# Kernel optimization log

Measured on AMD Instinct MI355X. Metric: run time of the kernel, lower is better.

Reference implementation:

```python
import jax, jax.numpy as jnp
import numpy as np

N, E, D = 50000, 800000, 128
NEG_SLOPE = 0.01  # torch LeakyReLU default


def _linear_params(key, fan_in, fan_out, bias=True):
    k1, k2 = jax.random.split(key)
    bound = 1.0 / np.sqrt(fan_in)
    W = jax.random.uniform(k1, (fan_in, fan_out), minval=-bound, maxval=bound, dtype=jnp.float32)
    if not bias:
        return W
    b = jax.random.uniform(k2, (fan_out,), minval=-bound, maxval=bound, dtype=jnp.float32)
    return W, b


def setup_inputs() -> dict:
    key = jax.random.key(0)
    ks = jax.random.split(key, 8)
    x = jax.random.normal(ks[0], (N, D), dtype=jnp.float32)
    edge_index = jax.random.randint(ks[1], (2, E), 0, N, dtype=jnp.int64)
    Wk, bk = _linear_params(ks[2], D, D)
    Wq, bq = _linear_params(ks[3], D, D)
    Wv, bv = _linear_params(ks[4], D, D)
    Wskip = _linear_params(ks[5], D, D, bias=False)  # lin_skip has bias=False
    b_conv = jnp.zeros((D,), dtype=jnp.float32)       # ResGatedGraphConv bias param
    Wlin, blin = _linear_params(ks[6], D, D)
    return {"x": x, "edge_index": edge_index, "Wk": Wk, "bk": bk, "Wq": Wq,
            "bq": bq, "Wv": Wv, "bv": bv, "Wskip": Wskip, "b_conv": b_conv,
            "Wlin": Wlin, "blin": blin}


def reference(x, edge_index, Wk, bk, Wq, bq, Wv, bv, Wskip, b_conv, Wlin, blin):
    src, dst = edge_index[0], edge_index[1]  # j -> i
    # dense projections on nodes (cheap), gather to edges (memory-bound)
    k = x @ Wk + bk          # [N, D] key of target
    q = x @ Wq + bq          # [N, D] query of source
    v = x @ Wv + bv          # [N, D] value of source
    gate = jax.nn.relu(k[dst] + q[src])      # act=ReLU() per module
    msg = gate * v[src]                       # [E, D]
    agg = jax.ops.segment_sum(msg, dst, num_segments=x.shape[0])  # scatter-add
    x1 = agg + x @ Wskip + b_conv            # root weight + bias
    x2 = jnp.where(x1 >= 0, x1, NEG_SLOPE * x1)  # LeakyReLU
    return x2 @ Wlin + blin
```

## Files before the change

kernel.cpp:

```cpp
#include <hip/hip_runtime.h>

#define DD 128

typedef __attribute__((ext_vector_type(8))) short bf16x8;
typedef __attribute__((ext_vector_type(4))) float f32x4;

__device__ inline unsigned short f2bf(float f) {
    unsigned int u = __float_as_uint(f);
    u += 0x7FFFu + ((u >> 16) & 1u);
    return (unsigned short)(u >> 16);
}
__device__ inline float bf2f(unsigned short s) {
    return __uint_as_float(((unsigned int)s) << 16);
}

template <typename T> __device__ inline T cvt(float f);
template <> __device__ inline float cvt<float>(float f) { return f; }
template <> __device__ inline unsigned short cvt<unsigned short>(float f) { return f2bf(f); }

template <typename T> __device__ inline float2 ld2(const T* p);
template <> __device__ inline float2 ld2<float>(const float* p) {
    return *reinterpret_cast<const float2*>(p);
}
template <> __device__ inline float2 ld2<unsigned short>(const unsigned short* p) {
    const ushort2 u = *reinterpret_cast<const ushort2*>(p);
    return make_float2(bf2f(u.x), bf2f(u.y));
}


__global__ __launch_bounds__(256) void split_w_kernel(
    const float* __restrict__ W0, const float* __restrict__ W1,
    const float* __restrict__ W2, const float* __restrict__ W3,
    const float* __restrict__ W4,
    unsigned short* __restrict__ whi)
{
    const int idx = blockIdx.x * 256 + threadIdx.x;
    if (idx >= 5 * 2048) return;
    const int mat  = idx >> 11;
    const int rem  = idx & 2047;
    const int ks   = rem >> 9;
    const int nt   = (rem >> 6) & 7;
    const int lane = rem & 63;
    const int lr = lane & 15, lg = lane >> 4;
    const float* __restrict__ W = mat == 0 ? W0 : mat == 1 ? W1 : mat == 2 ? W2
                                 : mat == 3 ? W3 : W4;
    const int n = nt * 16 + lr;
    bf16x8 h8;
#pragma unroll
    for (int r = 0; r < 8; ++r) {
        const int k = ks * 32 + lg * 8 + r;
        h8[r] = (short)f2bf(W[k * DD + n]);
    }
    *reinterpret_cast<bf16x8*>(&whi[(long)idx * 8]) = h8;
}

template <bool XFORM>
__device__ inline void stage_rows512(const float* __restrict__ src,
                                     const float* __restrict__ addv,
                                     int row0, int N, int t,
                                     unsigned short* __restrict__ ldsA)
{
    const int m  = t >> 3;
    const int gr = row0 + m;
#pragma unroll
    for (int j = 0; j < 2; ++j) {
        const int o = (t & 7) + j * 8;
        float v[8];
        if (gr < N) {
            const float4 a = *reinterpret_cast<const float4*>(&src[(long)gr * DD + o * 8]);
            const float4 b = *reinterpret_cast<const float4*>(&src[(long)gr * DD + o * 8 + 4]);
            v[0] = a.x; v[1] = a.y; v[2] = a.z; v[3] = a.w;
            v[4] = b.x; v[5] = b.y; v[6] = b.z; v[7] = b.w;
        } else {
#pragma unroll
            for (int e = 0; e < 8; ++e) v[e] = 0.f;
        }
        if (XFORM) {
#pragma unroll
            for (int e = 0; e < 8; ++e) {
                const float s = v[e] + addv[o * 8 + e];
                v[e] = s >= 0.f ? s : 0.01f * s;
            }
        }
        bf16x8 h8;
#pragma unroll
        for (int e = 0; e < 8; ++e) h8[e] = (short)f2bf(v[e]);
        const int rt   = m >> 4;
        const int ks   = o >> 2;
        const int lane = (m & 15) + (o & 3) * 16;
        const int base = ((rt * 4 + ks) * 64 + lane) * 8;
        *reinterpret_cast<bf16x8*>(&ldsA[base]) = h8;
    }
}

__global__ __launch_bounds__(512) void proj_mfma_kernel(
    const float* __restrict__ x,
    const unsigned short* __restrict__ whi,
    const float* __restrict__ bk, const float* __restrict__ bq,
    const float* __restrict__ bv,
    float* __restrict__ kbuf, unsigned short* __restrict__ qvpk,
    float* __restrict__ agg, int* __restrict__ deg, int N)
{
    __shared__ unsigned short ldsA[16 * 64 * 8];
    const int t = threadIdx.x;
    const int row0 = blockIdx.x * 64;

    const int gid = blockIdx.x * 512 + t;
    if (gid < N) deg[gid] = 0;

    stage_rows512<false>(x, nullptr, row0, N, t, ldsA);
    __syncthreads();

    const int wv   = t >> 6;
    const int mat  = wv >> 1;
    const int cc   = wv & 1;
    const int lane = t & 63;
    const int lr = lane & 15;
    const int lg = lane >> 4;
    const float* bias = (mat == 0) ? bk : (mat == 1) ? bq : (mat == 2) ? bv : nullptr;

    f32x4 acc[4][4];
#pragma unroll
    for (int rt = 0; rt < 4; ++rt)
#pragma unroll
        for (int ct = 0; ct < 4; ++ct) acc[rt][ct] = (f32x4){0.f, 0.f, 0.f, 0.f};

#pragma unroll
    for (int ks = 0; ks < 4; ++ks) {
        bf16x8 A[4];
#pragma unroll
        for (int rt = 0; rt < 4; ++rt)
            A[rt] = *reinterpret_cast<const bf16x8*>(&ldsA[((rt * 4 + ks) * 64 + lane) * 8]);
#pragma unroll
        for (int ct = 0; ct < 4; ++ct) {
            const long fb = ((long)((mat * 4 + ks) * 8 + (cc * 4 + ct)) * 64 + lane) * 8;
            const bf16x8 B = *reinterpret_cast<const bf16x8*>(&whi[fb]);
#pragma unroll
            for (int rt = 0; rt < 4; ++rt)
                acc[rt][ct] = __builtin_amdgcn_mfma_f32_16x16x32_bf16(A[rt], B, acc[rt][ct], 0, 0, 0);
        }
    }

#pragma unroll
    for (int ct = 0; ct < 4; ++ct) {
        const int n_l = cc * 64 + ct * 16 + lr;
        const float bv_ = bias ? bias[n_l] : 0.f;
#pragma unroll
        for (int rt = 0; rt < 4; ++rt) {
#pragma unroll
            for (int r = 0; r < 4; ++r) {
                const int m = row0 + rt * 16 + lg * 4 + r;
                if (m < N) {
                    const float val = acc[rt][ct][r] + bv_;
                    if      (mat == 0) kbuf [(long)m * 128 + n_l]         = val;
                    else if (mat == 1) qvpk [(long)m * 256 + 2 * n_l]     = f2bf(val);
                    else if (mat == 2) qvpk [(long)m * 256 + 2 * n_l + 1] = f2bf(val);
                    else               agg  [(long)m * 128 + n_l]         = val;
                }
            }
        }
    }
}

__global__ __launch_bounds__(512) void out_mfma_kernel(
    const float* agg, const float* __restrict__ bconv,
    const unsigned short* __restrict__ whi,
    const float* __restrict__ blin,
    float* out, int N)
{
    __shared__ unsigned short ldsA[16 * 64 * 8];
    const int t = threadIdx.x;
    const int row0 = blockIdx.x * 64;

    stage_rows512<true>(agg, bconv, row0, N, t, ldsA);
    __syncthreads();

    const int wv   = t >> 6;
    const int lane = t & 63;
    const int lr = lane & 15;
    const int lg = lane >> 4;

    f32x4 acc[4];
#pragma unroll
    for (int rt = 0; rt < 4; ++rt) acc[rt] = (f32x4){0.f, 0.f, 0.f, 0.f};

#pragma unroll
    for (int ks = 0; ks < 4; ++ks) {
        bf16x8 A[4];
#pragma unroll
        for (int rt = 0; rt < 4; ++rt)
            A[rt] = *reinterpret_cast<const bf16x8*>(&ldsA[((rt * 4 + ks) * 64 + lane) * 8]);
        const long fb = ((long)((16 + ks) * 8 + wv) * 64 + lane) * 8;
        const bf16x8 B = *reinterpret_cast<const bf16x8*>(&whi[fb]);
#pragma unroll
        for (int rt = 0; rt < 4; ++rt)
            acc[rt] = __builtin_amdgcn_mfma_f32_16x16x32_bf16(A[rt], B, acc[rt], 0, 0, 0);
    }

    const int n = wv * 16 + lr;
    const float bb = blin[n];
#pragma unroll
    for (int rt = 0; rt < 4; ++rt) {
#pragma unroll
        for (int r = 0; r < 4; ++r) {
            const int m = row0 + rt * 16 + lg * 4 + r;
            if (m < N) out[(long)m * 128 + n] = acc[rt][r] + bb;
        }
    }
}

__global__ __launch_bounds__(256) void gather_packed_kernel(
    const int* __restrict__ off, const int* __restrict__ deg,
    const int* __restrict__ ssrc,
    const float* __restrict__ kbuf, const unsigned short* __restrict__ qvpk,
    float* __restrict__ agg, int N)
{
    const int n = blockIdx.x * 4 + (threadIdx.x >> 6);
    if (n >= N) return;
    const int lane = threadIdx.x & 63;

    const int dg = deg[n];
    if (dg == 0) return;
    const int s0 = off[n];
    const int s1 = s0 + dg;

    const float2 k2 = *reinterpret_cast<const float2*>(&kbuf[(long)n * 128 + lane * 2]);
    float a0 = 0.f, a1 = 0.f, b0 = 0.f, b1 = 0.f;

    int e = s0;
    for (; e + 8 <= s1; e += 8) {
        int s[8];
#pragma unroll
        for (int j = 0; j < 8; ++j) s[j] = ssrc[e + j];
        ushort4 u[8];
#pragma unroll
        for (int j = 0; j < 8; ++j)
            u[j] = *reinterpret_cast<const ushort4*>(&qvpk[(long)s[j] * 256 + lane * 4]);
#pragma unroll
        for (int j = 0; j < 8; ++j) {
            const float q0 = bf2f(u[j].x), v0 = bf2f(u[j].y);
            const float q1 = bf2f(u[j].z), v1 = bf2f(u[j].w);
            if (j & 1) {
                b0 = fmaf(fmaxf(k2.x + q0, 0.f), v0, b0);
                b1 = fmaf(fmaxf(k2.y + q1, 0.f), v1, b1);
            } else {
                a0 = fmaf(fmaxf(k2.x + q0, 0.f), v0, a0);
                a1 = fmaf(fmaxf(k2.y + q1, 0.f), v1, a1);
            }
        }
    }
    for (; e < s1; ++e) {
        const int s = ssrc[e];
        const ushort4 u = *reinterpret_cast<const ushort4*>(&qvpk[(long)s * 256 + lane * 4]);
        a0 = fmaf(fmaxf(k2.x + bf2f(u.x), 0.f), bf2f(u.y), a0);
        a1 = fmaf(fmaxf(k2.y + bf2f(u.z), 0.f), bf2f(u.w), a1);
    }

    float2* ap = reinterpret_cast<float2*>(&agg[(long)n * 128 + lane * 2]);
    const float2 old = *ap;
    *ap = make_float2(old.x + a0 + b0, old.y + a1 + b1);
}

template <typename T>
__global__ __launch_bounds__(256) void proj_kernel(
    const float* __restrict__ x,
    const float* __restrict__ Wk, const float* __restrict__ bk,
    const float* __restrict__ Wq, const float* __restrict__ bq,
    const float* __restrict__ Wv, const float* __restrict__ bv,
    const float* __restrict__ Ws,
    T* __restrict__ kbuf, T* __restrict__ qvbuf, float* __restrict__ agg,
    int N)
{
    __shared__ float xt[32][DD];
    const int row0 = blockIdx.x * 32;
    const int t = threadIdx.x;

    for (int i = t; i < 32 * (DD / 4); i += 256) {
        const int r  = i >> 5;
        const int c4 = (i & 31) << 2;
        const int gr = row0 + r;
        float4 v = make_float4(0.f, 0.f, 0.f, 0.f);
        if (gr < N) v = *reinterpret_cast<const float4*>(&x[(long)gr * DD + c4]);
        *reinterpret_cast<float4*>(&xt[r][c4]) = v;
    }
    __syncthreads();

    const int c0 = t & 127;
    const int hi = t >> 7;
    const float* __restrict__ W0 = hi ? Wq : Wk;
    const float* __restrict__ W1 = hi ? Ws : Wv;
    const float b0 = hi ? bq[c0] : bk[c0];
    const float b1 = hi ? 0.f    : bv[c0];

    float acc0[32], acc1[32];
#pragma unroll
    for (int r = 0; r < 32; ++r) { acc0[r] = 0.f; acc1[r] = 0.f; }

    for (int k4 = 0; k4 < DD; k4 += 4) {
        const float w00 = W0[(k4 + 0) * DD + c0];
        const float w01 = W0[(k4 + 1) * DD + c0];
        const float w02 = W0[(k4 + 2) * DD + c0];
        const float w03 = W0[(k4 + 3) * DD + c0];
        const float w10 = W1[(k4 + 0) * DD + c0];
        const float w11 = W1[(k4 + 1) * DD + c0];
        const float w12 = W1[(k4 + 2) * DD + c0];
        const float w13 = W1[(k4 + 3) * DD + c0];
#pragma unroll
        for (int r = 0; r < 32; ++r) {
            const float4 xv = *reinterpret_cast<const float4*>(&xt[r][k4]);
            acc0[r] = fmaf(xv.x, w00, fmaf(xv.y, w01, fmaf(xv.z, w02, fmaf(xv.w, w03, acc0[r]))));
            acc1[r] = fmaf(xv.x, w10, fmaf(xv.y, w11, fmaf(xv.z, w12, fmaf(xv.w, w13, acc1[r]))));
        }
    }

#pragma unroll
    for (int r = 0; r < 32; ++r) {
        const long gr = row0 + r;
        if (gr < N) {
            if (hi == 0) {
                kbuf [gr * 128 + c0]       = cvt<T>(acc0[r] + b0);
                qvbuf[gr * 256 + 128 + c0] = cvt<T>(acc1[r] + b1);
            } else {
                qvbuf[gr * 256 + c0]       = cvt<T>(acc0[r] + b0);
                agg  [gr * 128 + c0]       = acc1[r];
            }
        }
    }
}

__global__ __launch_bounds__(256) void zero_kernel(int* __restrict__ p, int n) {
    const int i = blockIdx.x * 256 + threadIdx.x;
    if (i < n) p[i] = 0;
}

__global__ __launch_bounds__(256) void hist_kernel(
    const int* __restrict__ ei, int* __restrict__ deg, int E)
{
    const int e = blockIdx.x * 256 + threadIdx.x;
    if (e < E) atomicAdd(&deg[ei[E + e]], 1);
}

__global__ __launch_bounds__(1024) void scanA_kernel(
    const int* __restrict__ deg, int* __restrict__ off,
    int* __restrict__ bsum, int N)
{
    __shared__ int sm[1024];
    const int t = threadIdx.x;
    const int i = blockIdx.x * 1024 + t;
    const int v = (i < N) ? deg[i] : 0;
    int x = v;
    sm[t] = x;
    __syncthreads();
#pragma unroll
    for (int ofs = 1; ofs < 1024; ofs <<= 1) {
        const int y = (t >= ofs) ? sm[t - ofs] : 0;
        __syncthreads();
        x += y;
        sm[t] = x;
        __syncthreads();
    }
    if (i < N) off[i] = x - v;
    if (t == 1023) bsum[blockIdx.x] = x;
}

__global__ __launch_bounds__(1024) void scanB_kernel(int* __restrict__ bsum, int nb)
{
    __shared__ int sm[1024];
    const int t = threadIdx.x;
    const int v = (t < nb) ? bsum[t] : 0;
    int x = v;
    sm[t] = x;
    __syncthreads();
#pragma unroll
    for (int ofs = 1; ofs < 1024; ofs <<= 1) {
        const int y = (t >= ofs) ? sm[t - ofs] : 0;
        __syncthreads();
        x += y;
        sm[t] = x;
        __syncthreads();
    }
    if (t < nb) bsum[t] = x - v;
}

__global__ __launch_bounds__(256) void scanC_kernel(
    int* __restrict__ off, int* __restrict__ cursor,
    const int* __restrict__ bsum, int N)
{
    const int i = blockIdx.x * 256 + threadIdx.x;
    if (i < N) {
        const int o = off[i] + bsum[i >> 10];
        off[i]    = o;
        cursor[i] = o;
    }
}

__global__ __launch_bounds__(256) void scatter_kernel(
    const int* __restrict__ ei, int* __restrict__ cursor,
    int* __restrict__ ssrc, int E)
{
    const int e = blockIdx.x * 256 + threadIdx.x;
    if (e >= E) return;
    const int s = ei[e];
    const int d = ei[E + e];
    const int pos = atomicAdd(&cursor[d], 1);
    ssrc[pos] = s;
}

template <typename T>
__global__ __launch_bounds__(256) void gather_kernel(
    const int* __restrict__ off, const int* __restrict__ deg,
    const int* __restrict__ ssrc,
    const T* __restrict__ kbuf, const T* __restrict__ qvbuf,
    float* __restrict__ agg, int N)
{
    const int n = blockIdx.x * 4 + (threadIdx.x >> 6);
    if (n >= N) return;
    const int lane = threadIdx.x & 63;
    const int c = lane << 1;

    const int dg = deg[n];
    if (dg == 0) return;
    const int s0 = off[n];
    const int s1 = s0 + dg;

    const float2 k2 = ld2<T>(&kbuf[(long)n * 128 + c]);
    float a0 = 0.f, a1 = 0.f, b0 = 0.f, b1 = 0.f;

    int e = s0;
    for (; e + 4 <= s1; e += 4) {
        const long sa = ssrc[e + 0];
        const long sb = ssrc[e + 1];
        const long sc = ssrc[e + 2];
        const long sd = ssrc[e + 3];
        const float2 qa = ld2<T>(&qvbuf[sa * 256 + c]);
        const float2 va = ld2<T>(&qvbuf[sa * 256 + 128 + c]);
        const float2 qb = ld2<T>(&qvbuf[sb * 256 + c]);
        const float2 vb = ld2<T>(&qvbuf[sb * 256 + 128 + c]);
        const float2 qc = ld2<T>(&qvbuf[sc * 256 + c]);
        const float2 vc = ld2<T>(&qvbuf[sc * 256 + 128 + c]);
        const float2 qd = ld2<T>(&qvbuf[sd * 256 + c]);
        const float2 vd = ld2<T>(&qvbuf[sd * 256 + 128 + c]);
        a0 = fmaf(fmaxf(k2.x + qa.x, 0.f), va.x, a0);
        a1 = fmaf(fmaxf(k2.y + qa.y, 0.f), va.y, a1);
        b0 = fmaf(fmaxf(k2.x + qb.x, 0.f), vb.x, b0);
        b1 = fmaf(fmaxf(k2.y + qb.y, 0.f), vb.y, b1);
        a0 = fmaf(fmaxf(k2.x + qc.x, 0.f), vc.x, a0);
        a1 = fmaf(fmaxf(k2.y + qc.y, 0.f), vc.y, a1);
        b0 = fmaf(fmaxf(k2.x + qd.x, 0.f), vd.x, b0);
        b1 = fmaf(fmaxf(k2.y + qd.y, 0.f), vd.y, b1);
    }
    for (; e < s1; ++e) {
        const long s = ssrc[e];
        const float2 q = ld2<T>(&qvbuf[s * 256 + c]);
        const float2 v = ld2<T>(&qvbuf[s * 256 + 128 + c]);
        a0 = fmaf(fmaxf(k2.x + q.x, 0.f), v.x, a0);
        a1 = fmaf(fmaxf(k2.y + q.y, 0.f), v.y, a1);
    }

    float2* ap = reinterpret_cast<float2*>(&agg[(long)n * 128 + c]);
    const float2 old = *ap;
    *ap = make_float2(old.x + a0 + b0, old.y + a1 + b1);
}

template <typename T>
__global__ __launch_bounds__(256) void edge_kernel(
    const int* __restrict__ ei,
    const T* __restrict__ kbuf, const T* __restrict__ qvbuf,
    float* __restrict__ agg, int E)
{
    const int g = (blockIdx.x << 3) + (threadIdx.x >> 5);
    if (g >= E) return;
    const int lane = threadIdx.x & 31;
    const long src = (long)ei[g];
    const long dst = (long)ei[E + g];
    const int c = lane << 2;

    float kd[4], qs[4], vs[4];
    if constexpr (sizeof(T) == 4) {
        const float4 a = *reinterpret_cast<const float4*>(&kbuf[dst * 128 + c]);
        const float4 b = *reinterpret_cast<const float4*>(&qvbuf[src * 256 + c]);
        const float4 d = *reinterpret_cast<const float4*>(&qvbuf[src * 256 + 128 + c]);
        kd[0] = a.x; kd[1] = a.y; kd[2] = a.z; kd[3] = a.w;
        qs[0] = b.x; qs[1] = b.y; qs[2] = b.z; qs[3] = b.w;
        vs[0] = d.x; vs[1] = d.y; vs[2] = d.z; vs[3] = d.w;
    } else {
        const ushort4 a = *reinterpret_cast<const ushort4*>(&kbuf[dst * 128 + c]);
        const ushort4 b = *reinterpret_cast<const ushort4*>(&qvbuf[src * 256 + c]);
        const ushort4 d = *reinterpret_cast<const ushort4*>(&qvbuf[src * 256 + 128 + c]);
        kd[0] = bf2f(a.x); kd[1] = bf2f(a.y); kd[2] = bf2f(a.z); kd[3] = bf2f(a.w);
        qs[0] = bf2f(b.x); qs[1] = bf2f(b.y); qs[2] = bf2f(b.z); qs[3] = bf2f(b.w);
        vs[0] = bf2f(d.x); vs[1] = bf2f(d.y); vs[2] = bf2f(d.z); vs[3] = bf2f(d.w);
    }

    float* p = agg + dst * 128 + c;
#pragma unroll
    for (int j = 0; j < 4; ++j) {
        const float m = fmaxf(kd[j] + qs[j], 0.f) * vs[j];
        unsafeAtomicAdd(p + j, m);
    }
}

__global__ __launch_bounds__(64) void out_kernel(
    const float* agg, const float* __restrict__ bconv,
    const float* __restrict__ Wlin, const float* __restrict__ blin,
    float* out, int N)
{
    __shared__ float xt[32][DD];
    const int row0 = blockIdx.x * 32;
    const int t = threadIdx.x;

    for (int i = t; i < 32 * (DD / 4); i += 64) {
        const int r  = i >> 5;
        const int c4 = (i & 31) << 2;
        const int gr = row0 + r;
        float4 a = make_float4(0.f, 0.f, 0.f, 0.f);
        if (gr < N) a = *reinterpret_cast<const float4*>(&agg[(long)gr * DD + c4]);
        const float4 b = *reinterpret_cast<const float4*>(&bconv[c4]);
        float4 v;
        const float x0 = a.x + b.x; v.x = x0 >= 0.f ? x0 : 0.01f * x0;
        const float x1 = a.y + b.y; v.y = x1 >= 0.f ? x1 : 0.01f * x1;
        const float x2 = a.z + b.z; v.z = x2 >= 0.f ? x2 : 0.01f * x2;
        const float x3 = a.w + b.w; v.w = x3 >= 0.f ? x3 : 0.01f * x3;
        *reinterpret_cast<float4*>(&xt[r][c4]) = v;
    }
    __syncthreads();

    const int c0 = t;
    const int c1 = t + 64;
    float acc0[32], acc1[32];
#pragma unroll
    for (int r = 0; r < 32; ++r) { acc0[r] = 0.f; acc1[r] = 0.f; }

    for (int k4 = 0; k4 < DD; k4 += 4) {
        const float w00 = Wlin[(k4 + 0) * DD + c0];
        const float w01 = Wlin[(k4 + 1) * DD + c0];
        const float w02 = Wlin[(k4 + 2) * DD + c0];
        const float w03 = Wlin[(k4 + 3) * DD + c0];
        const float w10 = Wlin[(k4 + 0) * DD + c1];
        const float w11 = Wlin[(k4 + 1) * DD + c1];
        const float w12 = Wlin[(k4 + 2) * DD + c1];
        const float w13 = Wlin[(k4 + 3) * DD + c1];
#pragma unroll
        for (int r = 0; r < 32; ++r) {
            const float4 xv = *reinterpret_cast<const float4*>(&xt[r][k4]);
            acc0[r] = fmaf(xv.x, w00, fmaf(xv.y, w01, fmaf(xv.z, w02, fmaf(xv.w, w03, acc0[r]))));
            acc1[r] = fmaf(xv.x, w10, fmaf(xv.y, w11, fmaf(xv.z, w12, fmaf(xv.w, w13, acc1[r]))));
        }
    }

    const float bb0 = blin[c0];
    const float bb1 = blin[c1];
#pragma unroll
    for (int r = 0; r < 32; ++r) {
        const long gr = row0 + r;
        if (gr < N) {
            out[gr * DD + c0] = acc0[r] + bb0;
            out[gr * DD + c1] = acc1[r] + bb1;
        }
    }
}

extern "C" void kernel_launch(void* const* d_in, const int* in_sizes, int n_in,
                              void* d_out, int out_size, void* d_ws, size_t ws_size,
                              hipStream_t stream)
{
    const float* x     = (const float*)d_in[0];
    const int*   ei    = (const int*)d_in[1];
    const float* Wk    = (const float*)d_in[2];
    const float* bk    = (const float*)d_in[3];
    const float* Wq    = (const float*)d_in[4];
    const float* bq    = (const float*)d_in[5];
    const float* Wv    = (const float*)d_in[6];
    const float* bv    = (const float*)d_in[7];
    const float* Ws    = (const float*)d_in[8];
    const float* bconv = (const float*)d_in[9];
    const float* Wlin  = (const float*)d_in[10];
    const float* blin  = (const float*)d_in[11];

    const int N = in_sizes[0] / DD;
    const int E = in_sizes[1] / 2;

    float* aggf = (float*)d_out;
    const int nblk   = (N + 31) / 32;
    const int mblk   = (N + 63) / 64;
    const int eblk1  = (E + 255) / 256;
    const int nblk1  = (N + 255) / 256;
    const int gblk   = (N + 3) / 4;
    const int nchunks = (N + 1023) / 1024;

    const int bsum_pad = (nchunks + 255) & ~255;
    size_t csr_ints = (size_t)3 * N + bsum_pad + E;
    csr_ints = (csr_ints + 3) & ~(size_t)3;
    const size_t csr_bytes = csr_ints * sizeof(int);

    const size_t projPK   = (size_t)N * (128 * sizeof(float) + 256 * sizeof(unsigned short));
    const size_t projF32  = (size_t)N * 384 * sizeof(float);
    const size_t projBF16 = (size_t)N * 384 * sizeof(unsigned short);
    const size_t wsplit   = (size_t)5 * 2048 * 8 * sizeof(unsigned short);

    if (ws_size >= csr_bytes + projPK + wsplit) {
        int* deg    = (int*)d_ws;
        int* off    = deg + N;
        int* cursor = off + N;
        int* bsum   = cursor + N;
        int* ssrc   = bsum + bsum_pad;
        float* kbuf = (float*)((char*)d_ws + csr_bytes);
        unsigned short* qvpk = (unsigned short*)(kbuf + (size_t)N * 128);
        unsigned short* whi  = qvpk + (size_t)N * 256;

        split_w_kernel<<<40, 256, 0, stream>>>(Wk, Wq, Wv, Ws, Wlin, whi);
        proj_mfma_kernel<<<mblk, 512, 0, stream>>>(x, whi, bk, bq, bv,
                                                   kbuf, qvpk, aggf, deg, N);
        hist_kernel<<<eblk1, 256, 0, stream>>>(ei, deg, E);
        scanA_kernel<<<nchunks, 1024, 0, stream>>>(deg, off, bsum, N);
        scanB_kernel<<<1, 1024, 0, stream>>>(bsum, nchunks);
        scanC_kernel<<<nblk1, 256, 0, stream>>>(off, cursor, bsum, N);
        scatter_kernel<<<eblk1, 256, 0, stream>>>(ei, cursor, ssrc, E);
        gather_packed_kernel<<<gblk, 256, 0, stream>>>(off, deg, ssrc, kbuf, qvpk, aggf, N);
        out_mfma_kernel<<<mblk, 512, 0, stream>>>(aggf, bconv, whi, blin, (float*)d_out, N);
    } else if (ws_size >= csr_bytes + projF32) {
        int* deg    = (int*)d_ws;
        int* off    = deg + N;
        int* cursor = off + N;
        int* bsum   = cursor + N;
        int* ssrc   = bsum + bsum_pad;
        float* kbuf  = (float*)((char*)d_ws + csr_bytes);
        float* qvbuf = kbuf + (size_t)N * 128;

        proj_kernel<float><<<nblk, 256, 0, stream>>>(x, Wk, bk, Wq, bq, Wv, bv, Ws,
                                                     kbuf, qvbuf, aggf, N);
        zero_kernel<<<nblk1, 256, 0, stream>>>(deg, N);
        hist_kernel<<<eblk1, 256, 0, stream>>>(ei, deg, E);
        scanA_kernel<<<nchunks, 1024, 0, stream>>>(deg, off, bsum, N);
        scanB_kernel<<<1, 1024, 0, stream>>>(bsum, nchunks);
        scanC_kernel<<<nblk1, 256, 0, stream>>>(off, cursor, bsum, N);
        scatter_kernel<<<eblk1, 256, 0, stream>>>(ei, cursor, ssrc, E);
        gather_kernel<float><<<gblk, 256, 0, stream>>>(off, deg, ssrc, kbuf, qvbuf, aggf, N);
        out_kernel<<<nblk, 64, 0, stream>>>(aggf, bconv, Wlin, blin, (float*)d_out, N);
    } else if (ws_size >= csr_bytes + projBF16) {
        int* deg    = (int*)d_ws;
        int* off    = deg + N;
        int* cursor = off + N;
        int* bsum   = cursor + N;
        int* ssrc   = bsum + bsum_pad;
        unsigned short* kbuf  = (unsigned short*)((char*)d_ws + csr_bytes);
        unsigned short* qvbuf = kbuf + (size_t)N * 128;

        proj_kernel<unsigned short><<<nblk, 256, 0, stream>>>(x, Wk, bk, Wq, bq, Wv, bv, Ws,
                                                              kbuf, qvbuf, aggf, N);
        zero_kernel<<<nblk1, 256, 0, stream>>>(deg, N);
        hist_kernel<<<eblk1, 256, 0, stream>>>(ei, deg, E);
        scanA_kernel<<<nchunks, 1024, 0, stream>>>(deg, off, bsum, N);
        scanB_kernel<<<1, 1024, 0, stream>>>(bsum, nchunks);
        scanC_kernel<<<nblk1, 256, 0, stream>>>(off, cursor, bsum, N);
        scatter_kernel<<<eblk1, 256, 0, stream>>>(ei, cursor, ssrc, E);
        gather_kernel<unsigned short><<<gblk, 256, 0, stream>>>(off, deg, ssrc, kbuf, qvbuf, aggf, N);
        out_kernel<<<nblk, 64, 0, stream>>>(aggf, bconv, Wlin, blin, (float*)d_out, N);
    } else if (ws_size >= projBF16) {
        unsigned short* kbuf  = (unsigned short*)d_ws;
        unsigned short* qvbuf = kbuf + (size_t)N * 128;
        const int eblk8 = (E + 7) / 8;
        proj_kernel<unsigned short><<<nblk, 256, 0, stream>>>(x, Wk, bk, Wq, bq, Wv, bv, Ws,
                                                              kbuf, qvbuf, aggf, N);
        edge_kernel<unsigned short><<<eblk8, 256, 0, stream>>>(ei, kbuf, qvbuf, aggf, E);
        out_kernel<<<nblk, 64, 0, stream>>>(aggf, bconv, Wlin, blin, (float*)d_out, N);
    } else {
        hipMemsetAsync(d_out, 0, (size_t)out_size * sizeof(float), stream);
        return;
    }
}
```

Baseline: 229.6 us.

## Fuse CSR build stages to cut kernel launches in the packed MFMA path

Zeroing of degree and cursor arrays moves into the weight-split kernel. The degree histogram runs as extra blocks of the projection kernel, and the three scan kernels become one kernel whose last block, found with a done counter, scans the block sums. Scatter uses the local offset plus the block sum and a separate counter, which removes the scanC pass. This trims launches and small serialized kernels, but the histogram now contends with the projection blocks and the scan relies on atomic last-block detection.

```diff
diff --git a/kernel.cpp b/kernel.cpp
--- a/kernel.cpp
+++ b/kernel.cpp
@@ -32,9 +32,15 @@
     const float* __restrict__ W0, const float* __restrict__ W1,
     const float* __restrict__ W2, const float* __restrict__ W3,
     const float* __restrict__ W4,
-    unsigned short* __restrict__ whi)
-{
-    const int idx = blockIdx.x * 256 + threadIdx.x;
+    unsigned short* __restrict__ whi,
+    int* __restrict__ deg, int* __restrict__ cnt2, int* __restrict__ done,
+    int N)
+{
+    const int gid = blockIdx.x * 256 + threadIdx.x;
+    if (gid < N) { deg[gid] = 0; cnt2[gid] = 0; }
+    if (gid == 0) *done = 0;
+
+    const int idx = gid;
     if (idx >= 5 * 2048) return;
     const int mat  = idx >> 11;
     const int rem  = idx & 2047;
@@ -99,15 +105,20 @@
     const float* __restrict__ bk, const float* __restrict__ bq,
     const float* __restrict__ bv,
     float* __restrict__ kbuf, unsigned short* __restrict__ qvpk,
-    float* __restrict__ agg, int* __restrict__ deg, int N)
+    float* __restrict__ agg,
+    const int* __restrict__ ei, int* __restrict__ deg,
+    int projBlocks, int E, int N)
 {
     __shared__ unsigned short ldsA[16 * 64 * 8];
     const int t = threadIdx.x;
+
+    if (blockIdx.x >= projBlocks) {
+        const int e = (blockIdx.x - projBlocks) * 512 + t;
+        if (e < E) atomicAdd(&deg[ei[E + e]], 1);
+        return;
+    }
+
     const int row0 = blockIdx.x * 64;
-
-    const int gid = blockIdx.x * 512 + t;
-    if (gid < N) deg[gid] = 0;
-
     stage_rows512<false>(x, nullptr, row0, N, t, ldsA);
     __syncthreads();
 
@@ -162,6 +173,61 @@
     }
 }
 
+__global__ __launch_bounds__(1024) void scanAB_kernel(
+    const int* __restrict__ deg, int* __restrict__ off,
+    int* __restrict__ bsum, int* __restrict__ done, int N, int nb)
+{
+    __shared__ int sm[1024];
+    __shared__ int amLast;
+    const int t = threadIdx.x;
+    const int i = blockIdx.x * 1024 + t;
+    const int v = (i < N) ? deg[i] : 0;
+    int x = v;
+    sm[t] = x;
+    __syncthreads();
+#pragma unroll
+    for (int ofs = 1; ofs < 1024; ofs <<= 1) {
+        const int y = (t >= ofs) ? sm[t - ofs] : 0;
+        __syncthreads();
+        x += y;
+        sm[t] = x;
+        __syncthreads();
+    }
+    if (i < N) off[i] = x - v;
+    if (t == 1023) { bsum[blockIdx.x] = x; __threadfence(); }
+    __syncthreads();
+    if (t == 0) amLast = (atomicAdd(done, 1) == (int)gridDim.x - 1) ? 1 : 0;
+    __syncthreads();
+    if (!amLast) return;
+
+    const int vb = (t < nb) ? atomicAdd(&bsum[t], 0) : 0;
+    int xb = vb;
+    sm[t] = xb;
+    __syncthreads();
+#pragma unroll
+    for (int ofs = 1; ofs < 1024; ofs <<= 1) {
+        const int y = (t >= ofs) ? sm[t - ofs] : 0;
+        __syncthreads();
+        xb += y;
+        sm[t] = xb;
+        __syncthreads();
+    }
+    if (t < nb) bsum[t] = xb - vb;
+}
+
+__global__ __launch_bounds__(256) void scatter2_kernel(
+    const int* __restrict__ ei,
+    const int* __restrict__ off, const int* __restrict__ bsum,
+    int* __restrict__ cnt2, int* __restrict__ ssrc, int E)
+{
+    const int e = blockIdx.x * 256 + threadIdx.x;
+    if (e >= E) return;
+    const int s = ei[e];
+    const int d = ei[E + e];
+    const int pos = off[d] + bsum[d >> 10] + atomicAdd(&cnt2[d], 1);
+    ssrc[pos] = s;
+}
+
 __global__ __launch_bounds__(512) void out_mfma_kernel(
     const float* agg, const float* __restrict__ bconv,
     const unsigned short* __restrict__ whi,
@@ -210,8 +276,8 @@
 }
 
 __global__ __launch_bounds__(256) void gather_packed_kernel(
-    const int* __restrict__ off, const int* __restrict__ deg,
-    const int* __restrict__ ssrc,
+    const int* __restrict__ off, const int* __restrict__ bsum,
+    const int* __restrict__ deg, const int* __restrict__ ssrc,
     const float* __restrict__ kbuf, const unsigned short* __restrict__ qvpk,
     float* __restrict__ agg, int N)
 {
@@ -221,7 +287,7 @@
 
     const int dg = deg[n];
     if (dg == 0) return;
-    const int s0 = off[n];
+    const int s0 = off[n] + bsum[n >> 10];
     const int s1 = s0 + dg;
 
     const float2 k2 = *reinterpret_cast<const float2*>(&kbuf[(long)n * 128 + lane * 2]);
@@ -581,50 +647,57 @@
     const int E = in_sizes[1] / 2;
 
     float* aggf = (float*)d_out;
-    const int nblk   = (N + 31) / 32;
-    const int mblk   = (N + 63) / 64;
-    const int eblk1  = (E + 255) / 256;
-    const int nblk1  = (N + 255) / 256;
-    const int gblk   = (N + 3) / 4;
+    const int nblk    = (N + 31) / 32;
+    const int mblk    = (N + 63) / 64;
+    const int eblk1   = (E + 255) / 256;
+    const int nblk1   = (N + 255) / 256;
+    const int gblk    = (N + 3) / 4;
     const int nchunks = (N + 1023) / 1024;
+    const int hblk    = (E + 511) / 512;
 
     const int bsum_pad = (nchunks + 255) & ~255;
-    size_t csr_ints = (size_t)3 * N + bsum_pad + E;
-    csr_ints = (csr_ints + 3) & ~(size_t)3;
-    const size_t csr_bytes = csr_ints * sizeof(int);
+
+    size_t csrF_ints = (size_t)3 * N + bsum_pad + 256 + E;
+    csrF_ints = (csrF_ints + 3) & ~(size_t)3;
+    const size_t csrF_bytes = csrF_ints * sizeof(int);
+
+    size_t csrO_ints = (size_t)3 * N + bsum_pad + E;
+    csrO_ints = (csrO_ints + 3) & ~(size_t)3;
+    const size_t csrO_bytes = csrO_ints * sizeof(int);
 
     const size_t projPK   = (size_t)N * (128 * sizeof(float) + 256 * sizeof(unsigned short));
     const size_t projF32  = (size_t)N * 384 * sizeof(float);
     const size_t projBF16 = (size_t)N * 384 * sizeof(unsigned short);
     const size_t wsplit   = (size_t)5 * 2048 * 8 * sizeof(unsigned short);
 
-    if (ws_size >= csr_bytes + projPK + wsplit) {
+    if (ws_size >= csrF_bytes + projPK + wsplit) {
+        int* deg  = (int*)d_ws;
+        int* off  = deg + N;
+        int* cnt2 = off + N;
+        int* bsum = cnt2 + N;
+        int* done = bsum + bsum_pad;
+        int* ssrc = done + 256;
+        float* kbuf = (float*)((char*)d_ws + csrF_bytes);
+        unsigned short* qvpk = (unsigned short*)(kbuf + (size_t)N * 128);
+        unsigned short* whi  = qvpk + (size_t)N * 256;
+
+        const int swblk = (N + 255) / 256;
+        split_w_kernel<<<swblk, 256, 0, stream>>>(Wk, Wq, Wv, Ws, Wlin, whi,
+                                                  deg, cnt2, done, N);
+        proj_mfma_kernel<<<mblk + hblk, 512, 0, stream>>>(x, whi, bk, bq, bv,
+                                                          kbuf, qvpk, aggf,
+                                                          ei, deg, mblk, E, N);
+        scanAB_kernel<<<nchunks, 1024, 0, stream>>>(deg, off, bsum, done, N, nchunks);
+        scatter2_kernel<<<eblk1, 256, 0, stream>>>(ei, off, bsum, cnt2, ssrc, E);
+        gather_packed_kernel<<<gblk, 256, 0, stream>>>(off, bsum, deg, ssrc, kbuf, qvpk, aggf, N);
+        out_mfma_kernel<<<mblk, 512, 0, stream>>>(aggf, bconv, whi, blin, (float*)d_out, N);
+    } else if (ws_size >= csrO_bytes + projF32) {
         int* deg    = (int*)d_ws;
         int* off    = deg + N;
         int* cursor = off + N;
         int* bsum   = cursor + N;
         int* ssrc   = bsum + bsum_pad;
-        float* kbuf = (float*)((char*)d_ws + csr_bytes);
-        unsigned short* qvpk = (unsigned short*)(kbuf + (size_t)N * 128);
-        unsigned short* whi  = qvpk + (size_t)N * 256;
-
-        split_w_kernel<<<40, 256, 0, stream>>>(Wk, Wq, Wv, Ws, Wlin, whi);
-        proj_mfma_kernel<<<mblk, 512, 0, stream>>>(x, whi, bk, bq, bv,
-                                                   kbuf, qvpk, aggf, deg, N);
-        hist_kernel<<<eblk1, 256, 0, stream>>>(ei, deg, E);
-        scanA_kernel<<<nchunks, 1024, 0, stream>>>(deg, off, bsum, N);
-        scanB_kernel<<<1, 1024, 0, stream>>>(bsum, nchunks);
-        scanC_kernel<<<nblk1, 256, 0, stream>>>(off, cursor, bsum, N);
-        scatter_kernel<<<eblk1, 256, 0, stream>>>(ei, cursor, ssrc, E);
-        gather_packed_kernel<<<gblk, 256, 0, stream>>>(off, deg, ssrc, kbuf, qvpk, aggf, N);
-        out_mfma_kernel<<<mblk, 512, 0, stream>>>(aggf, bconv, whi, blin, (float*)d_out, N);
-    } else if (ws_size >= csr_bytes + projF32) {
-        int* deg    = (int*)d_ws;
-        int* off    = deg + N;
-        int* cursor = off + N;
-        int* bsum   = cursor + N;
-        int* ssrc   = bsum + bsum_pad;
-        float* kbuf  = (float*)((char*)d_ws + csr_bytes);
+        float* kbuf  = (float*)((char*)d_ws + csrO_bytes);
         float* qvbuf = kbuf + (size_t)N * 128;
 
         proj_kernel<float><<<nblk, 256, 0, stream>>>(x, Wk, bk, Wq, bq, Wv, bv, Ws,
@@ -637,13 +710,13 @@
         scatter_kernel<<<eblk1, 256, 0, stream>>>(ei, cursor, ssrc, E);
         gather_kernel<float><<<gblk, 256, 0, stream>>>(off, deg, ssrc, kbuf, qvbuf, aggf, N);
         out_kernel<<<nblk, 64, 0, stream>>>(aggf, bconv, Wlin, blin, (float*)d_out, N);
-    } else if (ws_size >= csr_bytes + projBF16) {
+    } else if (ws_size >= csrO_bytes + projBF16) {
         int* deg    = (int*)d_ws;
         int* off    = deg + N;
         int* cursor = off + N;
         int* bsum   = cursor + N;
         int* ssrc   = bsum + bsum_pad;
-        unsigned short* kbuf  = (unsigned short*)((char*)d_ws + csr_bytes);
+        unsigned short* kbuf  = (unsigned short*)((char*)d_ws + csrO_bytes);
         unsigned short* qvbuf = kbuf + (size_t)N * 128;
 
         proj_kernel<unsigned short><<<nblk, 256, 0, stream>>>(x, Wk, bk, Wq, bq, Wv, bv, Ws,
```

Result: no change. 229.0 us (-0.3%).
